# Optimization experiments

Hardware: AMD Instinct MI355X
Metric: run time of the kernel (lower is better)

Reference implementation:

```python
import jax, jax.numpy as jnp
import numpy as np

B, FIN, FOUT, H, W = 16, 16, 16, 384, 384
LAT, NMIX = 512, 8


def setup_inputs() -> dict:
    key = jax.random.key(0)
    ks = jax.random.split(key, 6)
    x = jax.random.normal(ks[0], (B, FIN, H, W), dtype=jnp.float32)
    lat = jax.random.normal(ks[1], (B, LAT), dtype=jnp.float32)
    # kernel_mix: [n_mix, fout, fin] (kernel_size=1 dims squeezed); xavier-normal-ish scale
    kernel_mix = jax.random.normal(ks[2], (NMIX, FOUT, FIN), dtype=jnp.float32) * np.sqrt(2.0 / (FIN + FOUT))
    bias_mix = jax.random.normal(ks[3], (NMIX, FOUT), dtype=jnp.float32) * np.sqrt(2.0 / (NMIX + FOUT))
    # dyna_mix Linear(lat_size, n_mix)
    w_dyn = jax.random.normal(ks[4], (NMIX, LAT), dtype=jnp.float32) * np.sqrt(1.0 / LAT)
    b_dyn = jax.random.normal(ks[5], (NMIX,), dtype=jnp.float32) * 0.01
    return {"x": x, "lat": lat, "kernel_mix": kernel_mix, "bias_mix": bias_mix,
            "w_dyn": w_dyn, "b_dyn": b_dyn}


def reference(x, lat, kernel_mix, bias_mix, w_dyn, b_dyn):
    # mixing coefficients per sample: [B, n_mix]
    mix = lat @ w_dyn.T + b_dyn
    # per-sample dynamic 1x1 kernel: [B, fout, fin]
    kernel = jnp.einsum('bm,moi->boi', mix, kernel_mix)
    # per-sample dynamic bias: [B, fout]
    bias = jnp.einsum('bm,mo->bo', mix, bias_mix)
    # grouped conv with batch*groups groups on 1x1 kernel == per-sample matmul over channels
    out = jnp.einsum('bihw,boi->bohw', x, kernel) + bias[:, :, None, None]
    return out
```

## Files before the change

kernel.cpp:

```cpp
#include <hip/hip_runtime.h>

#define BB   16
#define FIN  16
#define FOUT 16
#define HH   384
#define WW   384
#define LAT  512
#define NMIX 8
#define HW   (HH * WW)
#define HW4  (HW / 4)

typedef float f32x4 __attribute__((ext_vector_type(4)));

__global__ __launch_bounds__(256)
void mixconv_fused(const float* __restrict__ x,
                   const float* __restrict__ lat,
                   const float* __restrict__ kernel_mix,
                   const float* __restrict__ bias_mix,
                   const float* __restrict__ w_dyn,
                   const float* __restrict__ b_dyn,
                   float* __restrict__ out) {
    __shared__ float part[NMIX][32];
    __shared__ float mix_s[NMIX];
    __shared__ float ksh[FOUT][FIN];
    __shared__ float bsh[FOUT];

    const int t = threadIdx.x;
    const int b = blockIdx.y;

    const int p = blockIdx.x * 256 + t;
    const f32x4* xv = (const f32x4*)(x + (size_t)b * FIN * HW) + p;
    f32x4*       ov = (f32x4*)(out + (size_t)b * FOUT * HW) + p;

    f32x4 xi[FIN];
#pragma unroll
    for (int i = 0; i < FIN; ++i)
        xi[i] = __builtin_nontemporal_load(xv + (size_t)i * HW4);

    {
        const int m = t & (NMIX - 1);
        const int c = t >> 3;
        const f32x4* lv = (const f32x4*)(lat + (size_t)b * LAT + c * 16);
        const f32x4* wv = (const f32x4*)(w_dyn + (size_t)m * LAT + c * 16);
        float acc = 0.f;
#pragma unroll
        for (int j = 0; j < 4; ++j) {
            f32x4 a = lv[j], w = wv[j];
            acc += a.x * w.x + a.y * w.y + a.z * w.z + a.w * w.w;
        }
        part[m][c] = acc;
    }
    __syncthreads();
    if (t < NMIX) {
        float s = 0.f;
#pragma unroll
        for (int c = 0; c < 32; ++c) s += part[t][c];
        mix_s[t] = s + b_dyn[t];
    }
    __syncthreads();

    {
        float kacc = 0.f;
#pragma unroll
        for (int m = 0; m < NMIX; ++m)
            kacc += mix_s[m] * kernel_mix[m * FOUT * FIN + t];
        ((float*)ksh)[t] = kacc;
        if (t < FOUT) {
            float bacc = 0.f;
#pragma unroll
            for (int m = 0; m < NMIX; ++m)
                bacc += mix_s[m] * bias_mix[m * FOUT + t];
            bsh[t] = bacc;
        }
    }
    __syncthreads();

#pragma unroll
    for (int o = 0; o < FOUT; ++o) {
        const f32x4 k0 = *(const f32x4*)&ksh[o][0];
        const f32x4 k1 = *(const f32x4*)&ksh[o][4];
        const f32x4 k2 = *(const f32x4*)&ksh[o][8];
        const f32x4 k3 = *(const f32x4*)&ksh[o][12];
        const float bo = bsh[o];
        f32x4 acc = {bo, bo, bo, bo};
        acc += k0.x * xi[0];  acc += k0.y * xi[1];
        acc += k0.z * xi[2];  acc += k0.w * xi[3];
        acc += k1.x * xi[4];  acc += k1.y * xi[5];
        acc += k1.z * xi[6];  acc += k1.w * xi[7];
        acc += k2.x * xi[8];  acc += k2.y * xi[9];
        acc += k2.z * xi[10]; acc += k2.w * xi[11];
        acc += k3.x * xi[12]; acc += k3.y * xi[13];
        acc += k3.z * xi[14]; acc += k3.w * xi[15];
        __builtin_nontemporal_store(acc, ov + (size_t)o * HW4);
    }
}

extern "C" void kernel_launch(void* const* d_in, const int* in_sizes, int n_in,
                              void* d_out, int out_size, void* d_ws, size_t ws_size,
                              hipStream_t stream) {
    const float* x          = (const float*)d_in[0];
    const float* lat        = (const float*)d_in[1];
    const float* kernel_mix = (const float*)d_in[2];
    const float* bias_mix   = (const float*)d_in[3];
    const float* w_dyn      = (const float*)d_in[4];
    const float* b_dyn      = (const float*)d_in[5];
    float* out = (float*)d_out;

    dim3 grid(HW4 / 256, BB);
    mixconv_fused<<<grid, dim3(256), 0, stream>>>(
        x, lat, kernel_mix, bias_mix, w_dyn, b_dyn, out);
}
```

Measured before the change: 255.3 us.

## Split per-sample weight mixing into a prologue kernel and drop block barriers

The mixing-coefficient and dynamic kernel/bias computation, which every block of the fused kernel repeated with three __syncthreads, moves into a small kernel that runs once per sample and writes to workspace. The main kernel loads the precomputed 272 floats per sample, and each wavefront keeps its own LDS copy so no block-wide barrier is needed. This removes redundant work and barrier stalls, at the cost of an extra kernel launch and a serial dependency. It relies on wavefront-synchronous LDS visibility without an explicit barrier.

Measured after the change: 257.8 us. Within noise of the previous version (+1.0%).

```diff
diff --git a/kernel.cpp b/kernel.cpp
--- a/kernel.cpp
+++ b/kernel.cpp
@@ -9,33 +9,21 @@
 #define NMIX 8
 #define HW   (HH * WW)
 #define HW4  (HW / 4)
+#define WSTRIDE 272
 
 typedef float f32x4 __attribute__((ext_vector_type(4)));
 
 __global__ __launch_bounds__(256)
-void mixconv_fused(const float* __restrict__ x,
-                   const float* __restrict__ lat,
-                   const float* __restrict__ kernel_mix,
-                   const float* __restrict__ bias_mix,
-                   const float* __restrict__ w_dyn,
-                   const float* __restrict__ b_dyn,
-                   float* __restrict__ out) {
+void mixconv_weights(const float* __restrict__ lat,
+                     const float* __restrict__ kernel_mix,
+                     const float* __restrict__ bias_mix,
+                     const float* __restrict__ w_dyn,
+                     const float* __restrict__ b_dyn,
+                     float* __restrict__ ws) {
     __shared__ float part[NMIX][32];
     __shared__ float mix_s[NMIX];
-    __shared__ float ksh[FOUT][FIN];
-    __shared__ float bsh[FOUT];
-
     const int t = threadIdx.x;
-    const int b = blockIdx.y;
-
-    const int p = blockIdx.x * 256 + t;
-    const f32x4* xv = (const f32x4*)(x + (size_t)b * FIN * HW) + p;
-    f32x4*       ov = (f32x4*)(out + (size_t)b * FOUT * HW) + p;
-
-    f32x4 xi[FIN];
-#pragma unroll
-    for (int i = 0; i < FIN; ++i)
-        xi[i] = __builtin_nontemporal_load(xv + (size_t)i * HW4);
+    const int b = blockIdx.x;
 
     {
         const int m = t & (NMIX - 1);
@@ -59,28 +47,60 @@
     }
     __syncthreads();
 
-    {
-        float kacc = 0.f;
+    float kacc = 0.f;
+#pragma unroll
+    for (int m = 0; m < NMIX; ++m)
+        kacc += mix_s[m] * kernel_mix[m * FOUT * FIN + t];
+    ws[b * WSTRIDE + t] = kacc;
+    if (t < FOUT) {
+        float bacc = 0.f;
 #pragma unroll
         for (int m = 0; m < NMIX; ++m)
-            kacc += mix_s[m] * kernel_mix[m * FOUT * FIN + t];
-        ((float*)ksh)[t] = kacc;
-        if (t < FOUT) {
-            float bacc = 0.f;
+            bacc += mix_s[m] * bias_mix[m * FOUT + t];
+        ws[b * WSTRIDE + 256 + t] = bacc;
+    }
+}
+
+__global__ __launch_bounds__(256)
+void mixconv_main(const float* __restrict__ x,
+                  const float* __restrict__ wk,
+                  float* __restrict__ out) {
+    __shared__ float wsh[4][WSTRIDE];
+    const int t    = threadIdx.x;
+    const int wid  = t >> 6;
+    const int lane = t & 63;
+    const int b    = blockIdx.y;
+
+    float wv[5];
 #pragma unroll
-            for (int m = 0; m < NMIX; ++m)
-                bacc += mix_s[m] * bias_mix[m * FOUT + t];
-            bsh[t] = bacc;
-        }
+    for (int j = 0; j < 5; ++j) {
+        const int idx = lane + j * 64;
+        if (idx < WSTRIDE) wv[j] = wk[b * WSTRIDE + idx];
     }
-    __syncthreads();
+
+    const int p = blockIdx.x * 256 + t;
+    const f32x4* xv = (const f32x4*)(x + (size_t)b * FIN * HW) + p;
+    f32x4*       ov = (f32x4*)(out + (size_t)b * FOUT * HW) + p;
+
+    f32x4 xi[FIN];
+#pragma unroll
+    for (int i = 0; i < FIN; ++i)
+        xi[i] = __builtin_nontemporal_load(xv + (size_t)i * HW4);
 
 #pragma unroll
+    for (int j = 0; j < 5; ++j) {
+        const int idx = lane + j * 64;
+        if (idx < WSTRIDE) wsh[wid][idx] = wv[j];
+    }
+
+    const float* ksh = &wsh[wid][0];
+    const float* bsh = &wsh[wid][256];
+#pragma unroll
     for (int o = 0; o < FOUT; ++o) {
-        const f32x4 k0 = *(const f32x4*)&ksh[o][0];
-        const f32x4 k1 = *(const f32x4*)&ksh[o][4];
-        const f32x4 k2 = *(const f32x4*)&ksh[o][8];
-        const f32x4 k3 = *(const f32x4*)&ksh[o][12];
+        const f32x4 k0 = *(const f32x4*)&ksh[o * 16 + 0];
+        const f32x4 k1 = *(const f32x4*)&ksh[o * 16 + 4];
+        const f32x4 k2 = *(const f32x4*)&ksh[o * 16 + 8];
+        const f32x4 k3 = *(const f32x4*)&ksh[o * 16 + 12];
         const float bo = bsh[o];
         f32x4 acc = {bo, bo, bo, bo};
         acc += k0.x * xi[0];  acc += k0.y * xi[1];
@@ -105,8 +125,11 @@
     const float* w_dyn      = (const float*)d_in[4];
     const float* b_dyn      = (const float*)d_in[5];
     float* out = (float*)d_out;
+    float* ws  = (float*)d_ws;
+
+    mixconv_weights<<<dim3(BB), dim3(256), 0, stream>>>(
+        lat, kernel_mix, bias_mix, w_dyn, b_dyn, ws);
 
     dim3 grid(HW4 / 256, BB);
-    mixconv_fused<<<grid, dim3(256), 0, stream>>>(
-        x, lat, kernel_mix, bias_mix, w_dyn, b_dyn, out);
+    mixconv_main<<<grid, dim3(256), 0, stream>>>(x, ws, out);
 }
```
